# Optimization experiments

Hardware: AMD Instinct MI355X
Metric: run time of the kernel (lower is better)

Reference implementation:

```python
import jax, jax.numpy as jnp
import numpy as np


def _lap_min(a):
    """Jonker-Volgenant style Hungarian on cost matrix a (n x m, n <= m), minimizing.
    Returns (rows, cols) of the optimal assignment (len n)."""
    n, m = a.shape
    INF = 1e18
    u = np.zeros(n + 1)
    v = np.zeros(m + 1)
    p = np.zeros(m + 1, dtype=np.int64)   # p[j] = row matched to column j (1-based), 0 = free
    way = np.zeros(m + 1, dtype=np.int64)
    for i in range(1, n + 1):
        p[0] = i
        j0 = 0
        minv = np.full(m + 1, INF)
        used = np.zeros(m + 1, dtype=bool)
        while True:
            used[j0] = True
            i0 = p[j0]
            cur = a[i0 - 1] - u[i0] - v[1:]
            free = ~used[1:]
            upd = free & (cur < minv[1:])
            minv[1:][upd] = cur[upd]
            way[1:][upd] = j0
            mv = np.where(free, minv[1:], INF)
            j1 = int(np.argmin(mv)) + 1
            delta = mv[j1 - 1]
            idx = np.where(used)[0]
            u[p[idx]] += delta
            v[idx] -= delta
            minv[1:][free] -= delta
            j0 = j1
            if p[j0] == 0:
                break
        while j0:
            j1 = way[j0]
            p[j0] = p[j1]
            j0 = j1
    rows = p[1:] - 1
    cols = np.arange(m)
    sel = rows >= 0
    return rows[sel], cols[sel]


def _hungarian(scores, n1s, n2s):
    """Batched max-score LAP on scores[b, :n1, :n2]; returns binary [B,N,M] assignment."""
    B, N, M = scores.shape
    out = np.zeros((B, N, M), dtype=np.float32)
    for b in range(B):
        n, m = int(n1s[b]), int(n2s[b])
        sub = -scores[b, :n, :m].astype(np.float64)
        if n <= m:
            rows, cols = _lap_min(sub)
        else:
            cols, rows = _lap_min(sub.T)
        out[b, rows, cols] = 1.0
    return out


def _loss(pred, gt, dis, pred_ns, gt_ns):
    ali = dis + gt
    ali = jnp.where(ali > 1.0, jnp.float32(0.9), ali)
    p = ali * pred
    g = ali * gt
    N = pred.shape[1]
    M = pred.shape[2]
    mask = (jnp.arange(N)[None, :, None] < pred_ns[:, None, None]) & \
           (jnp.arange(M)[None, None, :] < gt_ns[:, None, None])
    # torch F.binary_cross_entropy clamps log terms at -100
    bce = -(g * jnp.clip(jnp.log(p), -100.0, None)
            + (1.0 - g) * jnp.clip(jnp.log1p(-p), -100.0, None))
    loss = jnp.sum(jnp.where(mask, bce, 0.0))
    n_sum = jnp.sum(pred_ns).astype(pred.dtype)
    return loss / n_sum


def setup_inputs() -> dict:
    B, N = 2048, 64
    key = jax.random.key(0)
    k1, _ = jax.random.split(key)
    # soft doubly-stochastic-ish prediction, strictly inside (0,1)
    pred = 0.01 + 0.98 * jax.random.uniform(k1, (B, N, N), dtype=jnp.float32)
    rng = np.random.default_rng(0)
    ns = rng.integers(N // 2, N + 1, size=B).astype(np.int32)
    gt = np.zeros((B, N, N), dtype=np.float32)
    for b in range(B):
        n = int(ns[b])
        perm = rng.permutation(n)
        gt[b, np.arange(n), perm] = 1.0
    return {"pred_perm": pred, "gt_perm": jnp.asarray(gt),
            "pred_ns": jnp.asarray(ns), "gt_ns": jnp.asarray(ns)}


def reference(pred_perm, gt_perm, pred_ns, gt_ns):
    # Hungarian is discrete (non-differentiable) and runs on host, as in the original
    dis = jnp.asarray(_hungarian(np.asarray(pred_perm),
                                 np.asarray(pred_ns), np.asarray(gt_ns)))
    return _loss(pred_perm, gt_perm, dis, pred_ns, gt_ns)
```

## Files before the change

### kernel.cpp

```cpp
#include <hip/hip_runtime.h>
#include <hip/hip_bf16.h>

#define NMAX 64

typedef float f32x32 __attribute__((ext_vector_type(32)));

__device__ __forceinline__ double readlane_d(double x, int l) {
    const int lo = __builtin_amdgcn_readlane(__double2loint(x), l);
    const int hi = __builtin_amdgcn_readlane(__double2hiint(x), l);
    return __hiloint2double(hi, lo);
}
template <int CTRL>
__device__ __forceinline__ float dpp_fmin(float x) {
    const int t = __builtin_amdgcn_update_dpp(0, __float_as_int(x), CTRL, 0xF, 0xF, true);
    return fminf(x, __int_as_float(t));
}
template <int CTRL>
__device__ __forceinline__ double dpp_add_step(double x) {
    const int lo = __builtin_amdgcn_update_dpp(0, __double2loint(x), CTRL, 0xF, 0xF, true);
    const int hi = __builtin_amdgcn_update_dpp(0, __double2hiint(x), CTRL, 0xF, 0xF, true);
    return x + __hiloint2double(hi, lo);
}
__device__ __forceinline__ double wave_sum_f64(double x) {
    x = dpp_add_step<0xB1>(x);  x = dpp_add_step<0x4E>(x);
    x = dpp_add_step<0x141>(x); x = dpp_add_step<0x140>(x);
    x = dpp_add_step<0x142>(x); x = dpp_add_step<0x143>(x);
    return readlane_d(x, 63);
}
__device__ __forceinline__ unsigned sel_u32(unsigned long long m, unsigned a, unsigned b) {
    unsigned r;
    asm("v_cndmask_b32 %0, %1, %2, %3" : "=v"(r) : "v"(b), "v"(a), "s"(m));
    return r;
}
__device__ __forceinline__ float sel_f32(unsigned long long m, float a, float b) {
    return __int_as_float((int)sel_u32(m, (unsigned)__float_as_int(a),
                                          (unsigned)__float_as_int(b)));
}
__device__ __forceinline__ int sel_i32(unsigned long long m, int a, int b) {
    return (int)sel_u32(m, (unsigned)a, (unsigned)b);
}

__global__ __launch_bounds__(64, 2) void hung_loss_kernel(
    const float* __restrict__ pred, const float* __restrict__ gt,
    const int* __restrict__ n1s, const int* __restrict__ n2s,
    double* __restrict__ partial)
{
    const int b = blockIdx.x;
    const int lane = threadIdx.x & 63;
    const float* __restrict__ predb = pred + (size_t)b * NMAX * NMAX;
    const float* __restrict__ gtb   = gt   + (size_t)b * NMAX * NMAX;
    const int n1 = n1s[b];
    const int n2 = n2s[b];
    const bool trans = (n1 > n2);
    const int n = trans ? n2 : n1;
    const int m = trans ? n1 : n2;
    const float FINF = __int_as_float(0x7f800000);
    const float FNINF = __int_as_float(0xff800000);

    f32x32 alo, ahi;
    if (!trans) {
        #pragma unroll
        for (int r = 0; r < 32; ++r) alo[r] = predb[r * NMAX + lane];
        #pragma unroll
        for (int r = 0; r < 32; ++r) ahi[r] = predb[(r + 32) * NMAX + lane];
    } else {
        #pragma unroll
        for (int r = 0; r < 32; ++r) alo[r] = predb[lane * NMAX + r];
        #pragma unroll
        for (int r = 0; r < 32; ++r) ahi[r] = predb[lane * NMAX + 32 + r];
    }
    if (lane >= m) {
        #pragma unroll
        for (int r = 0; r < 32; ++r) { alo[r] = FNINF; ahi[r] = FNINF; }
    }

    float v;
    int am = 0;
    {
        float mx = FNINF;
        #pragma unroll
        for (int r = 0; r < 32; ++r) {
            const bool take = (r < n) && (alo[r] > mx);
            mx = take ? alo[r] : mx;
            am = take ? r : am;
        }
        #pragma unroll
        for (int r = 0; r < 32; ++r) {
            const bool take = ((r + 32) < n) && (ahi[r] > mx);
            mx = take ? ahi[r] : mx;
            am = take ? (r + 32) : am;
        }
        v = (lane < m) ? (-mx) : 0.0f;
    }

    __shared__ int mincol[NMAX];
    mincol[lane] = 127;
    __syncthreads();
    if (lane < m) atomicMin(&mincol[am], lane);
    __syncthreads();
    const bool matched = (lane < m) && (mincol[am] == lane);
    int p = matched ? (am + 1) : 0;
    const unsigned long long rowsM =
        __ballot((lane < n) && (mincol[lane] != 127));
    unsigned long long freerows =
        (~rowsM) & ((n == 64) ? ~0ull : ((1ull << n) - 1ull));

    float u = 0.0f;
    float uent = 0.0f;
    float dsel = 0.0f;

    while (freerows) {
        const int i = __ffsll(freerows);
        freerows &= freerows - 1;
        unsigned long long um = 0ull;
        unsigned long long rowm = 1ull << (i - 1);
        float d = FINF;
        int way = 0;
        int vj0 = 0;
        int i0 = i;
        float sui = __int_as_float(__builtin_amdgcn_readlane(__float_as_int(u), i - 1));
        float sdelta = 0.0f;
        uent = sel_f32(rowm, 0.0f, uent);
        int rr = i - 1;
        float aval;
        { const float aL = alo[rr & 31], aH = ahi[rr & 31]; aval = (rr & 32) ? aH : aL; }
        int j1f = 0;
        for (int guard = 0; guard < NMAX; ++guard) {
            const float t   = aval + sui;
            const float t2  = (-t) - v;
            const float cur = t2 + sdelta;
            const bool lt = cur < d;
            way = lt ? vj0 : way;
            d = fminf(d, cur);
            float red = d;
            red = dpp_fmin<0xB1>(red);
            red = dpp_fmin<0x4E>(red);
            red = dpp_fmin<0x141>(red);
            red = dpp_fmin<0x140>(red);
            red = dpp_fmin<0x142>(red);
            red = dpp_fmin<0x143>(red);
            const int Hb = __builtin_amdgcn_readlane(__float_as_int(red), 63);
            const float H = __int_as_float(Hb);
            const unsigned long long tie = __ballot(d == H);
            const int j1 = __ffsll(tie);
            i0 = __builtin_amdgcn_readlane(p, j1 - 1);
            const unsigned long long mj = 1ull << (j1 - 1);
            dsel = sel_f32(mj, d, dsel);
            d    = sel_f32(mj, FINF, d);
            sdelta = H;
            if (i0 == 0) { j1f = j1; break; }
            um |= mj;
            rowm |= 1ull << (i0 - 1);
            sui = __int_as_float(__builtin_amdgcn_readlane(__float_as_int(u), i0 - 1));
            uent = sel_f32(1ull << (i0 - 1), sdelta, uent);
            rr = i0 - 1;
            { const float aL = alo[rr & 31], aH = ahi[rr & 31]; aval = (rr & 32) ? aH : aL; }
            aval = __int_as_float((int)sel_u32(um, 0xFF800000u, __float_as_int(aval)));
            vj0 = j1;
        }
        const float DT = sdelta;
        v = sel_f32(um,   v + (dsel - DT), v);
        u = sel_f32(rowm, u + (DT - uent), u);
        int j0 = j1f;
        while (j0 > 0) {
            const int j1w = __builtin_amdgcn_readlane(way, j0 - 1);
            const int newp = (j1w == 0) ? i : __builtin_amdgcn_readlane(p, j1w - 1);
            p = sel_i32(1ull << (j0 - 1), newp, p);
            j0 = j1w;
        }
    }

    double lsum = 0.0;
    if (!trans) {
        #pragma unroll
        for (int i2 = 0; i2 < NMAX; ++i2) {
            const float pv = (i2 < 32) ? alo[i2] : ahi[i2 - 32];
            const float gv = gtb[i2 * NMAX + lane];
            const float dis = (p == i2 + 1) ? 1.0f : 0.0f;
            float ali = dis + gv;
            if (ali > 1.0f) ali = 0.9f;
            const float pp = ali * pv;
            const float gg = ali * gv;
            const float lp  = fmaxf(logf(pp),    -100.0f);
            const float l1p = fmaxf(log1pf(-pp), -100.0f);
            const float bce = -(gg * lp + (1.0f - gg) * l1p);
            if (i2 < n1 && lane < n2) lsum += (double)bce;
        }
    } else {
        for (int i2 = 0; i2 < NMAX; ++i2) {
            const float pv = predb[i2 * NMAX + lane];
            const float gv = gtb[i2 * NMAX + lane];
            const int pi = __builtin_amdgcn_readlane(p, i2);
            const float dis = (pi - 1 == lane) ? 1.0f : 0.0f;
            float ali = dis + gv;
            if (ali > 1.0f) ali = 0.9f;
            const float pp = ali * pv;
            const float gg = ali * gv;
            const float lp  = fmaxf(logf(pp),    -100.0f);
            const float l1p = fmaxf(log1pf(-pp), -100.0f);
            const float bce = -(gg * lp + (1.0f - gg) * l1p);
            if (i2 < n1 && lane < n2) lsum += (double)bce;
        }
    }
    const double tsum = wave_sum_f64(lsum);
    if (lane == 0) partial[b] = tsum;
}

__global__ __launch_bounds__(256) void finalize_kernel(
    const double* __restrict__ partial, const int* __restrict__ n1s,
    float* __restrict__ out, int B)
{
    __shared__ double sred[256];
    __shared__ int    nred[256];
    const int t = threadIdx.x;
    double s = 0.0;
    int ns = 0;
    for (int bb = t; bb < B; bb += 256) { s += partial[bb]; ns += n1s[bb]; }
    sred[t] = s; nred[t] = ns;
    __syncthreads();
    for (int off = 128; off >= 1; off >>= 1) {
        if (t < off) { sred[t] += sred[t + off]; nred[t] += nred[t + off]; }
        __syncthreads();
    }
    if (t == 0) out[0] = (float)sred[0] / (float)nred[0];
}

extern "C" void kernel_launch(void* const* d_in, const int* in_sizes, int n_in,
                              void* d_out, int out_size, void* d_ws, size_t ws_size,
                              hipStream_t stream) {
    const float* pred = (const float*)d_in[0];
    const float* gt   = (const float*)d_in[1];
    const int* n1s    = (const int*)d_in[2];
    const int* n2s    = (const int*)d_in[3];
    float* out = (float*)d_out;
    double* partial = (double*)d_ws;
    const int B = in_sizes[2];

    hung_loss_kernel<<<B, 64, 0, stream>>>(pred, gt, n1s, n2s, partial);
    finalize_kernel<<<1, 256, 0, stream>>>(partial, n1s, out, B);
}
```

Before: 128.3 us.

## Stage cost matrix in padded LDS and split the augmenting-step min-reduction

The 64x64 cost matrix is no longer held as two 32-wide register vectors. It is loaded with float4 reads into a padded shared-memory tile (stride 65), and any transpose is done on the way in. The inner Hungarian loop reads the current row from LDS and runs two independent DPP min reductions, one over the old d and one over the new row, then combines them. This takes the reduction off the critical path that follows the cost update. Unused columns are excluded through an initial 'used' mask instead of -inf filling. The aim is to cut VGPR pressure so more waves fit, and to shorten the serial latency of each step, at the cost of an LDS load in every iteration.

```diff
diff --git a/kernel.cpp b/kernel.cpp
--- a/kernel.cpp
+++ b/kernel.cpp
@@ -2,13 +2,15 @@
 #include <hip/hip_bf16.h>
 
 #define NMAX 64
-
-typedef float f32x32 __attribute__((ext_vector_type(32)));
+#define LDA 65
 
 __device__ __forceinline__ double readlane_d(double x, int l) {
     const int lo = __builtin_amdgcn_readlane(__double2loint(x), l);
     const int hi = __builtin_amdgcn_readlane(__double2hiint(x), l);
     return __hiloint2double(hi, lo);
+}
+__device__ __forceinline__ float readlane_f(float x, int l) {
+    return __int_as_float(__builtin_amdgcn_readlane(__float_as_int(x), l));
 }
 template <int CTRL>
 __device__ __forceinline__ float dpp_fmin(float x) {
@@ -26,6 +28,12 @@
     x = dpp_add_step<0x141>(x); x = dpp_add_step<0x140>(x);
     x = dpp_add_step<0x142>(x); x = dpp_add_step<0x143>(x);
     return readlane_d(x, 63);
+}
+__device__ __forceinline__ float dpp_min6(float x) {
+    x = dpp_fmin<0xB1>(x);  x = dpp_fmin<0x4E>(x);
+    x = dpp_fmin<0x141>(x); x = dpp_fmin<0x140>(x);
+    x = dpp_fmin<0x142>(x); x = dpp_fmin<0x143>(x);
+    return x;
 }
 __device__ __forceinline__ unsigned sel_u32(unsigned long long m, unsigned a, unsigned b) {
     unsigned r;
@@ -54,48 +62,43 @@
     const bool trans = (n1 > n2);
     const int n = trans ? n2 : n1;
     const int m = trans ? n1 : n2;
-    const float FINF = __int_as_float(0x7f800000);
+    const float FINF  = __int_as_float(0x7f800000);
     const float FNINF = __int_as_float(0xff800000);
 
-    f32x32 alo, ahi;
-    if (!trans) {
+    __shared__ float A[NMAX * LDA];
+    __shared__ int mincol[NMAX];
+    mincol[lane] = 127;
+    {
+        const float4* p4 = (const float4*)predb;
         #pragma unroll
-        for (int r = 0; r < 32; ++r) alo[r] = predb[r * NMAX + lane];
-        #pragma unroll
-        for (int r = 0; r < 32; ++r) ahi[r] = predb[(r + 32) * NMAX + lane];
-    } else {
-        #pragma unroll
-        for (int r = 0; r < 32; ++r) alo[r] = predb[lane * NMAX + r];
-        #pragma unroll
-        for (int r = 0; r < 32; ++r) ahi[r] = predb[lane * NMAX + 32 + r];
-    }
-    if (lane >= m) {
-        #pragma unroll
-        for (int r = 0; r < 32; ++r) { alo[r] = FNINF; ahi[r] = FNINF; }
-    }
+        for (int it = 0; it < 16; ++it) {
+            const float4 val = p4[it * 64 + lane];
+            const int r = it * 4 + (lane >> 4);
+            const int c = (lane & 15) * 4;
+            if (!trans) {
+                A[r * LDA + c + 0] = val.x; A[r * LDA + c + 1] = val.y;
+                A[r * LDA + c + 2] = val.z; A[r * LDA + c + 3] = val.w;
+            } else {
+                A[(c + 0) * LDA + r] = val.x; A[(c + 1) * LDA + r] = val.y;
+                A[(c + 2) * LDA + r] = val.z; A[(c + 3) * LDA + r] = val.w;
+            }
+        }
+    }
+    __syncthreads();
 
     float v;
     int am = 0;
     {
         float mx = FNINF;
-        #pragma unroll
-        for (int r = 0; r < 32; ++r) {
-            const bool take = (r < n) && (alo[r] > mx);
-            mx = take ? alo[r] : mx;
+        for (int r = 0; r < n; ++r) {
+            const float a = A[r * LDA + lane];
+            const bool take = a > mx;
+            mx = take ? a : mx;
             am = take ? r : am;
         }
-        #pragma unroll
-        for (int r = 0; r < 32; ++r) {
-            const bool take = ((r + 32) < n) && (ahi[r] > mx);
-            mx = take ? ahi[r] : mx;
-            am = take ? (r + 32) : am;
-        }
         v = (lane < m) ? (-mx) : 0.0f;
     }
 
-    __shared__ int mincol[NMAX];
-    mincol[lane] = 127;
-    __syncthreads();
     if (lane < m) atomicMin(&mincol[am], lane);
     __syncthreads();
     const bool matched = (lane < m) && (mincol[am] == lane);
@@ -108,57 +111,46 @@
     float u = 0.0f;
     float uent = 0.0f;
     float dsel = 0.0f;
+    const unsigned long long fake = (m < 64) ? (~0ull << m) : 0ull;
 
     while (freerows) {
         const int i = __ffsll(freerows);
         freerows &= freerows - 1;
-        unsigned long long um = 0ull;
+        unsigned long long um = fake;
         unsigned long long rowm = 1ull << (i - 1);
         float d = FINF;
         int way = 0;
         int vj0 = 0;
         int i0 = i;
-        float sui = __int_as_float(__builtin_amdgcn_readlane(__float_as_int(u), i - 1));
-        float sdelta = 0.0f;
+        float s = 0.0f - readlane_f(u, i - 1);
         uent = sel_f32(rowm, 0.0f, uent);
-        int rr = i - 1;
-        float aval;
-        { const float aL = alo[rr & 31], aH = ahi[rr & 31]; aval = (rr & 32) ? aH : aL; }
         int j1f = 0;
+        float DT = 0.0f;
         for (int guard = 0; guard < NMAX; ++guard) {
-            const float t   = aval + sui;
-            const float t2  = (-t) - v;
-            const float cur = t2 + sdelta;
+            float a = A[(i0 - 1) * LDA + lane];
+            const float redD = dpp_min6(d);
+            a = __int_as_float((int)sel_u32(um, 0xFF800000u, __float_as_int(a)));
+            const float r_ = (-a) - v;
+            const float redR = dpp_min6(r_);
+            const float H = readlane_f(fminf(redD, redR + s), 63);
+            const float cur = r_ + s;
+            const float dn = fminf(d, cur);
+            const unsigned long long tie = __ballot(dn == H);
+            const int j1 = __ffsll(tie);
+            const int i0n = __builtin_amdgcn_readlane(p, j1 - 1);
+            const unsigned long long mj = 1ull << (j1 - 1);
             const bool lt = cur < d;
-            way = lt ? vj0 : way;
-            d = fminf(d, cur);
-            float red = d;
-            red = dpp_fmin<0xB1>(red);
-            red = dpp_fmin<0x4E>(red);
-            red = dpp_fmin<0x141>(red);
-            red = dpp_fmin<0x140>(red);
-            red = dpp_fmin<0x142>(red);
-            red = dpp_fmin<0x143>(red);
-            const int Hb = __builtin_amdgcn_readlane(__float_as_int(red), 63);
-            const float H = __int_as_float(Hb);
-            const unsigned long long tie = __ballot(d == H);
-            const int j1 = __ffsll(tie);
-            i0 = __builtin_amdgcn_readlane(p, j1 - 1);
-            const unsigned long long mj = 1ull << (j1 - 1);
-            dsel = sel_f32(mj, d, dsel);
-            d    = sel_f32(mj, FINF, d);
-            sdelta = H;
-            if (i0 == 0) { j1f = j1; break; }
+            way  = lt ? vj0 : way;
+            dsel = sel_f32(mj, dn, dsel);
+            d    = sel_f32(mj, FINF, dn);
+            if (i0n == 0) { j1f = j1; DT = H; break; }
             um |= mj;
-            rowm |= 1ull << (i0 - 1);
-            sui = __int_as_float(__builtin_amdgcn_readlane(__float_as_int(u), i0 - 1));
-            uent = sel_f32(1ull << (i0 - 1), sdelta, uent);
-            rr = i0 - 1;
-            { const float aL = alo[rr & 31], aH = ahi[rr & 31]; aval = (rr & 32) ? aH : aL; }
-            aval = __int_as_float((int)sel_u32(um, 0xFF800000u, __float_as_int(aval)));
+            rowm |= 1ull << (i0n - 1);
+            uent = sel_f32(1ull << (i0n - 1), H, uent);
+            s = H - readlane_f(u, i0n - 1);
+            i0 = i0n;
             vj0 = j1;
         }
-        const float DT = sdelta;
         v = sel_f32(um,   v + (dsel - DT), v);
         u = sel_f32(rowm, u + (DT - uent), u);
         int j0 = j1f;
@@ -172,9 +164,8 @@
 
     double lsum = 0.0;
     if (!trans) {
-        #pragma unroll
         for (int i2 = 0; i2 < NMAX; ++i2) {
-            const float pv = (i2 < 32) ? alo[i2] : ahi[i2 - 32];
+            const float pv = A[i2 * LDA + lane];
             const float gv = gtb[i2 * NMAX + lane];
             const float dis = (p == i2 + 1) ? 1.0f : 0.0f;
             float ali = dis + gv;
```

Result: slower. 153.4 us (+19.5%).

## Add auction-style augmenting row reduction and packed-key argmin in Hungarian loop

Applied to the files above, without the earlier changes.

Adds a preliminary augmenting row reduction phase, as in Jonker-Volgenant, that assigns free rows using the smallest and second-smallest reduced costs, bounded at 128 steps. This should leave fewer rows for the full shortest-path search. The shortest-path loop now packs a truncated float value with the lane index into one unsigned key, so a single DPP min-reduction returns both the minimum and its argmin, replacing the float min, ballot and ffs sequence. Masking off the low 6 mantissa bits and clamping at zero can change tie-breaking and precision, which risks picking a non-optimal assignment on near-ties.

```diff
diff --git a/kernel.cpp b/kernel.cpp
--- a/kernel.cpp
+++ b/kernel.cpp
@@ -10,10 +10,19 @@
     const int hi = __builtin_amdgcn_readlane(__double2hiint(x), l);
     return __hiloint2double(hi, lo);
 }
+__device__ __forceinline__ float readlane_f(float x, int l) {
+    return __int_as_float(__builtin_amdgcn_readlane(__float_as_int(x), l));
+}
 template <int CTRL>
-__device__ __forceinline__ float dpp_fmin(float x) {
-    const int t = __builtin_amdgcn_update_dpp(0, __float_as_int(x), CTRL, 0xF, 0xF, true);
-    return fminf(x, __int_as_float(t));
+__device__ __forceinline__ unsigned dpp_umin(unsigned x) {
+    const unsigned t = (unsigned)__builtin_amdgcn_update_dpp(0, (int)x, CTRL, 0xF, 0xF, true);
+    return x < t ? x : t;
+}
+__device__ __forceinline__ unsigned dpp_umin6(unsigned x) {
+    x = dpp_umin<0xB1>(x);  x = dpp_umin<0x4E>(x);
+    x = dpp_umin<0x141>(x); x = dpp_umin<0x140>(x);
+    x = dpp_umin<0x142>(x); x = dpp_umin<0x143>(x);
+    return x;
 }
 template <int CTRL>
 __device__ __forceinline__ double dpp_add_step(double x) {
@@ -38,6 +47,10 @@
 }
 __device__ __forceinline__ int sel_i32(unsigned long long m, int a, int b) {
     return (int)sel_u32(m, (unsigned)a, (unsigned)b);
+}
+__device__ __forceinline__ float mat_get(const f32x32& lo, const f32x32& hi, int rr) {
+    const float aL = lo[rr & 31], aH = hi[rr & 31];
+    return (rr & 32) ? aH : aL;
 }
 
 __global__ __launch_bounds__(64, 2) void hung_loss_kernel(
@@ -54,7 +67,7 @@
     const bool trans = (n1 > n2);
     const int n = trans ? n2 : n1;
     const int m = trans ? n1 : n2;
-    const float FINF = __int_as_float(0x7f800000);
+    const float FINF  = __int_as_float(0x7f800000);
     const float FNINF = __int_as_float(0xff800000);
 
     f32x32 alo, ahi;
@@ -108,6 +121,38 @@
     float u = 0.0f;
     float uent = 0.0f;
     float dsel = 0.0f;
+    const unsigned VMASK = 0xFFFFFFC0u;
+
+    {
+        int steps = 0;
+        while (freerows && steps < 128) {
+            ++steps;
+            const int i = __ffsll(freerows);
+            freerows &= freerows - 1;
+            const float a = mat_get(alo, ahi, i - 1);
+            float r_ = (0.0f - a) - v;
+            r_ = fmaxf(r_, 0.0f);
+            const unsigned key1 = (__float_as_uint(r_) & VMASK) | (unsigned)lane;
+            const unsigned K1 = (unsigned)__builtin_amdgcn_readlane((int)dpp_umin6(key1), 63);
+            const int j1 = (int)(K1 & 63u) + 1;
+            const unsigned key2 = sel_u32(1ull << (j1 - 1), 0xFFFFFFFFu, key1);
+            const unsigned K2 = (unsigned)__builtin_amdgcn_readlane((int)dpp_umin6(key2), 63);
+            const unsigned u1b = K1 & VMASK, u2b = K2 & VMASK;
+            const float u2f = __uint_as_float(u2b);
+            int jt = j1;
+            int i0k = __builtin_amdgcn_readlane(p, j1 - 1);
+            if (u1b < u2b) {
+                const float u1f = __uint_as_float(u1b);
+                v = sel_f32(1ull << (j1 - 1), v - (u2f - u1f), v);
+            } else if (i0k != 0) {
+                jt = (int)(K2 & 63u) + 1;
+                i0k = __builtin_amdgcn_readlane(p, jt - 1);
+            }
+            p = sel_i32(1ull << (jt - 1), i, p);
+            u = sel_f32(1ull << (i - 1), u2f, u);
+            if (i0k != 0) freerows |= 1ull << (i0k - 1);
+        }
+    }
 
     while (freerows) {
         const int i = __ffsll(freerows);
@@ -117,48 +162,34 @@
         float d = FINF;
         int way = 0;
         int vj0 = 0;
-        int i0 = i;
-        float sui = __int_as_float(__builtin_amdgcn_readlane(__float_as_int(u), i - 1));
-        float sdelta = 0.0f;
+        float s = 0.0f - readlane_f(u, i - 1);
         uent = sel_f32(rowm, 0.0f, uent);
-        int rr = i - 1;
-        float aval;
-        { const float aL = alo[rr & 31], aH = ahi[rr & 31]; aval = (rr & 32) ? aH : aL; }
+        float aval = mat_get(alo, ahi, i - 1);
         int j1f = 0;
+        float DT = 0.0f;
         for (int guard = 0; guard < NMAX; ++guard) {
-            const float t   = aval + sui;
-            const float t2  = (-t) - v;
-            const float cur = t2 + sdelta;
+            const float r_ = (0.0f - aval) - v;
+            const float cur = fmaxf(r_ + s, 0.0f);
+            const float dn = fminf(d, cur);
+            const unsigned key = (__float_as_uint(dn) & VMASK) | (unsigned)lane;
+            const unsigned K = (unsigned)__builtin_amdgcn_readlane((int)dpp_umin6(key), 63);
+            const int j1 = (int)(K & 63u) + 1;
+            const int i0n = __builtin_amdgcn_readlane(p, j1 - 1);
+            const float H = __uint_as_float(K & VMASK);
+            const unsigned long long mj = 1ull << (j1 - 1);
             const bool lt = cur < d;
-            way = lt ? vj0 : way;
-            d = fminf(d, cur);
-            float red = d;
-            red = dpp_fmin<0xB1>(red);
-            red = dpp_fmin<0x4E>(red);
-            red = dpp_fmin<0x141>(red);
-            red = dpp_fmin<0x140>(red);
-            red = dpp_fmin<0x142>(red);
-            red = dpp_fmin<0x143>(red);
-            const int Hb = __builtin_amdgcn_readlane(__float_as_int(red), 63);
-            const float H = __int_as_float(Hb);
-            const unsigned long long tie = __ballot(d == H);
-            const int j1 = __ffsll(tie);
-            i0 = __builtin_amdgcn_readlane(p, j1 - 1);
-            const unsigned long long mj = 1ull << (j1 - 1);
-            dsel = sel_f32(mj, d, dsel);
-            d    = sel_f32(mj, FINF, d);
-            sdelta = H;
-            if (i0 == 0) { j1f = j1; break; }
+            way  = lt ? vj0 : way;
+            dsel = sel_f32(mj, dn, dsel);
+            d    = sel_f32(mj, FINF, dn);
+            if (i0n == 0) { j1f = j1; DT = H; break; }
             um |= mj;
-            rowm |= 1ull << (i0 - 1);
-            sui = __int_as_float(__builtin_amdgcn_readlane(__float_as_int(u), i0 - 1));
-            uent = sel_f32(1ull << (i0 - 1), sdelta, uent);
-            rr = i0 - 1;
-            { const float aL = alo[rr & 31], aH = ahi[rr & 31]; aval = (rr & 32) ? aH : aL; }
+            rowm |= 1ull << (i0n - 1);
+            uent = sel_f32(1ull << (i0n - 1), H, uent);
+            s = H - readlane_f(u, i0n - 1);
+            aval = mat_get(alo, ahi, i0n - 1);
             aval = __int_as_float((int)sel_u32(um, 0xFF800000u, __float_as_int(aval)));
             vj0 = j1;
         }
-        const float DT = sdelta;
         v = sel_f32(um,   v + (dsel - DT), v);
         u = sel_f32(rowm, u + (DT - uent), u);
         int j0 = j1f;
```

New measurement: 111.2 us. -13.3%, faster.
